# Performance work log

Hardware: AMD Instinct MI355X
Metric: run time of the kernel (lower is better)

## Reference

```python
import jax, jax.numpy as jnp
import numpy as np

B, N, DIM, H, D = 1, 1024, 512, 8, 64
BC, BS, K, W = 16, 16, 8, 256   # compress blk, selection blk, top-k blocks, sliding window
C = N // BC                     # number of compression / selection blocks
SCALE = D ** -0.5
EPS = 1e-6
NEG = -1e30


def rmsnorm(x):
    return x * jax.lax.rsqrt(jnp.mean(x * x, axis=-1, keepdims=True) + EPS)


def rope(x):  # x: [B,H,N,D], GPT-NeoX style half rotation
    half = D // 2
    inv = 1.0 / (10000.0 ** (jnp.arange(half, dtype=jnp.float32) / half))
    ang = jnp.arange(x.shape[2], dtype=jnp.float32)[:, None] * inv
    cos, sin = jnp.cos(ang), jnp.sin(ang)
    x1, x2 = x[..., :half], x[..., half:]
    return jnp.concatenate([x1 * cos - x2 * sin, x2 * cos + x1 * sin], axis=-1).astype(x.dtype)


def setup_inputs():
    key = jax.random.key(0)
    ks = jax.random.split(key, 24)
    w = lambda k, shape, fan: jax.random.normal(k, shape, jnp.float32) * (fan ** -0.5)
    return {
        'x':  jax.random.normal(ks[0], (B, N, DIM), jnp.float32),
        've': jax.random.normal(ks[1], (B, N, DIM), jnp.float32),
        'x0': jax.random.normal(ks[2], (B, N, DIM), jnp.float32),
        'lambdas': jnp.array([1.0, 0.0], jnp.float32),
        'Wq': w(ks[3], (DIM, H * D), DIM),
        'Wk': w(ks[4], (DIM, H * D), DIM),
        'Wv': w(ks[5], (DIM, H * D), DIM),
        'Wo': w(ks[6], (H * D, DIM), H * D),
        'Wg': w(ks[7], (DIM, 3 * H), DIM),
        'k_pos': w(ks[8], (H, BC, D), D),
        'v_pos': w(ks[9], (H, BC, D), D),
        'Wck': w(ks[10], (BC * D, D), BC * D),
        'bck': jnp.zeros((D,), jnp.float32),
        'Wcv': w(ks[11], (BC * D, D), BC * D),
        'bcv': jnp.zeros((D,), jnp.float32),
        'k_mem': w(ks[12], (H, 1, D), D),
        'v_mem': w(ks[13], (H, 1, D), D),
        'W1': w(ks[14], (DIM, 4 * DIM), DIM),
        'W2': w(ks[15], (4 * DIM, DIM), 4 * DIM),
    }


def _nsa_attn(xn, Wq, Wk, Wv, Wo, Wg, k_pos, v_pos, Wck, bck, Wcv, bcv, k_mem, v_mem):
    q = (xn @ Wq).reshape(B, N, H, D).transpose(0, 2, 1, 3)   # [B,H,N,D]
    k = (xn @ Wk).reshape(B, N, H, D).transpose(0, 2, 1, 3)
    v = (xn @ Wv).reshape(B, N, H, D).transpose(0, 2, 1, 3)
    q, k = rope(q), rope(k)
    i_idx = jnp.arange(N)

    # ---- compressed branch: pool kv into blocks via learned linear + intra-block pos emb ----
    kb = k.reshape(B, H, C, BC, D) + k_pos[None, :, None]
    vb = v.reshape(B, H, C, BC, D) + v_pos[None, :, None]
    ck = kb.reshape(B, H, C, BC * D) @ Wck + bck              # [B,H,C,D]
    cv = vb.reshape(B, H, C, BC * D) @ Wcv + bcv
    ckf = jnp.concatenate([jnp.broadcast_to(k_mem[None], (B, H, 1, D)), ck], axis=2)
    cvf = jnp.concatenate([jnp.broadcast_to(v_mem[None], (B, H, 1, D)), cv], axis=2)
    csim = jnp.einsum('bhid,bhjd->bhij', q, ckf) * SCALE      # [B,H,N,C+1]
    past = ((jnp.arange(C) + 1) * BC - 1)[None, :] < i_idx[:, None]   # block fully in the past
    cmask = jnp.concatenate([jnp.ones((N, 1), bool), past], axis=1)   # mem kv always visible
    cattn = jax.nn.softmax(jnp.where(cmask[None, None], csim, NEG), axis=-1)
    c_out = jnp.einsum('bhij,bhjd->bhid', cattn, cvf)

    # ---- fine selection branch: top-K blocks by compressed attention importance ----
    imp = jnp.where(past[None, None], cattn[..., 1:], NEG)    # [B,H,N,C]
    vals, sel = jax.lax.top_k(imp, K)                         # [B,H,N,K]
    valid = vals >= 0.0                                       # drop picks among masked blocks
    kb_f = k.reshape(B, H, C, BS, D)
    vb_f = v.reshape(B, H, C, BS, D)
    k_sel = jnp.take_along_axis(kb_f[:, :, None], sel[..., None, None], axis=3)  # [B,H,N,K,BS,D]
    v_sel = jnp.take_along_axis(vb_f[:, :, None], sel[..., None, None], axis=3)
    own = i_idx // BS                                         # query's own block, causal inside
    k_fine = jnp.concatenate([k_sel, kb_f[:, :, own][:, :, :, None]], axis=3)    # [B,H,N,K+1,BS,D]
    v_fine = jnp.concatenate([v_sel, vb_f[:, :, own][:, :, :, None]], axis=3)
    offs = jnp.arange(BS)
    m_sel = (sel[..., None] * BS + offs <= i_idx[None, None, :, None, None]) & valid[..., None]
    m_own = jnp.broadcast_to((own[:, None] * BS + offs <= i_idx[:, None])[None, None, :, None], (B, H, N, 1, BS))
    m_fine = jnp.concatenate([m_sel, m_own], axis=3)
    fsim = jnp.where(m_fine, jnp.einsum('bhnd,bhnksd->bhnks', q, k_fine) * SCALE, NEG)
    fattn = jax.nn.softmax(fsim.reshape(B, H, N, (K + 1) * BS), axis=-1).reshape(B, H, N, K + 1, BS)
    f_out = jnp.einsum('bhnks,bhnksd->bhnd', fattn, v_fine)

    # ---- sliding window branch ----
    smask = (i_idx[None, :] <= i_idx[:, None]) & (i_idx[:, None] - i_idx[None, :] < W)
    ssim = jnp.where(smask[None, None], jnp.einsum('bhid,bhjd->bhij', q, k) * SCALE, NEG)
    s_out = jnp.einsum('bhij,bhjd->bhid', jax.nn.softmax(ssim, axis=-1), v)

    # ---- per-head sigmoid gates combine the three strategies ----
    gates = jax.nn.sigmoid(xn @ Wg).reshape(B, N, H, 3).transpose(0, 2, 1, 3)  # [B,H,N,3]
    o = gates[..., 0:1] * c_out + gates[..., 1:2] * f_out + gates[..., 2:3] * s_out
    return o.transpose(0, 2, 1, 3).reshape(B, N, H * D) @ Wo


def reference(x, ve, x0, lambdas, Wq, Wk, Wv, Wo, Wg, k_pos, v_pos, Wck, bck, Wcv, bcv, k_mem, v_mem, W1, W2):
    # ve is accepted by NSABlock.forward but never consumed in this block
    x = lambdas[0] * x + lambdas[1] * x0
    x = x + _nsa_attn(rmsnorm(x), Wq, Wk, Wv, Wo, Wg, k_pos, v_pos, Wck, bck, Wcv, bcv, k_mem, v_mem)
    x = x + jnp.square(jax.nn.relu(rmsnorm(x) @ W1)) @ W2
    return x
```

## Files before the change

kernel.cpp:

```cpp
#include <hip/hip_runtime.h>
#include <math.h>

#define NTOK 1024
#define DIMM 512
#define NH 8
#define HD 64
#define BCB 16
#define BSB 16
#define KSEL 8
#define WWIN 256
#define CBLK 64
#define SCALE 0.125f
#define EPSV 1e-6f
#define NEGV -1e30f

typedef short bf16x8 __attribute__((ext_vector_type(8)));
typedef float f32x4 __attribute__((ext_vector_type(4)));

__device__ inline ushort f2b(float f) {
  union { float f; unsigned int u; } c; c.f = f;
  unsigned int u = c.u;
  return (ushort)((u + 0x7FFFu + ((u >> 16) & 1u)) >> 16);
}
__device__ inline float b2f(ushort h) {
  union { unsigned int u; float f; } c; c.u = ((unsigned int)h) << 16;
  return c.f;
}

__device__ inline float wred_max(float v) {
#pragma unroll
  for (int off = 1; off < 64; off <<= 1) v = fmaxf(v, __shfl_xor(v, off));
  return v;
}
__device__ inline float wred_sum(float v) {
#pragma unroll
  for (int off = 1; off < 64; off <<= 1) v += __shfl_xor(v, off);
  return v;
}

struct WtrDesc { const float* src; ushort* dh; ushort* dl; int K; int Nsrc; int Npad; };
struct WtrPack { WtrDesc d[9]; int cum[9]; };

__global__ void __launch_bounds__(256)
k_pre(WtrPack pk, const float* __restrict__ x, const float* __restrict__ x0,
      const float* __restrict__ lam, float* __restrict__ xr,
      ushort* __restrict__ xnh, ushort* __restrict__ xnl) {
  if ((int)blockIdx.x < pk.cum[8]) {
    int gb = blockIdx.x;
    int e = 0;
    while (gb >= pk.cum[e]) e++;
    int start = e ? pk.cum[e - 1] : 0;
    WtrDesc dd = pk.d[e];
    int local = gb - start;
    int XT = dd.Npad >> 5;
    int bx = local % XT, by = local / XT;
    __shared__ float t[32][33];
    int n0 = bx * 32, k0 = by * 32;
    int tx = threadIdx.x & 31, ty = threadIdx.x >> 5;
#pragma unroll
    for (int i = 0; i < 32; i += 8)
      t[ty + i][tx] = (n0 + tx < dd.Nsrc)
          ? dd.src[(size_t)(k0 + ty + i) * dd.Nsrc + n0 + tx] : 0.f;
    __syncthreads();
#pragma unroll
    for (int i = 0; i < 32; i += 8) {
      float vv = t[tx][ty + i];
      ushort h = f2b(vv);
      size_t di = (size_t)(n0 + ty + i) * dd.K + k0 + tx;
      dd.dh[di] = h;
      if (dd.dl) dd.dl[di] = f2b(vv - b2f(h));
    }
  } else {
    int row = blockIdx.x - pk.cum[8], tid = threadIdx.x;
    float l0 = lam[0], l1 = lam[1];
    size_t b = (size_t)row * DIMM;
    float a0 = l0 * x[b + tid]       + l1 * x0[b + tid];
    float a1 = l0 * x[b + tid + 256] + l1 * x0[b + tid + 256];
    xr[b + tid] = a0; xr[b + tid + 256] = a1;
    float ss = a0 * a0 + a1 * a1;
    __shared__ float sm[8];
    for (int o = 32; o > 0; o >>= 1) ss += __shfl_down(ss, o);
    int lane = tid & 63, wid = tid >> 6;
    if (lane == 0) sm[wid] = ss;
    __syncthreads();
    if (tid == 0) {
      float s = sm[0] + sm[1] + sm[2] + sm[3];
      sm[0] = rsqrtf(s / (float)DIMM + EPSV);
    }
    __syncthreads();
    float r = sm[0];
    float v0 = a0 * r, v1 = a1 * r;
    ushort h0 = f2b(v0), h1 = f2b(v1);
    xnh[b + tid] = h0;        xnh[b + tid + 256] = h1;
    xnl[b + tid] = f2b(v0 - b2f(h0));
    xnl[b + tid + 256] = f2b(v1 - b2f(h1));
  }
}

__global__ void __launch_bounds__(256)
k_rms_bf(const float* __restrict__ xr, const float* __restrict__ p0,
         const float* __restrict__ p1, float* __restrict__ outb,
         ushort* __restrict__ y) {
  int row = blockIdx.x, tid = threadIdx.x;
  size_t b = (size_t)row * DIMM;
  float a0 = xr[b + tid]       + p0[b + tid]       + p1[b + tid];
  float a1 = xr[b + tid + 256] + p0[b + tid + 256] + p1[b + tid + 256];
  outb[b + tid] = a0; outb[b + tid + 256] = a1;
  float ss = a0 * a0 + a1 * a1;
  __shared__ float sm[8];
  for (int o = 32; o > 0; o >>= 1) ss += __shfl_down(ss, o);
  int lane = tid & 63, wid = tid >> 6;
  if (lane == 0) sm[wid] = ss;
  __syncthreads();
  if (tid == 0) {
    float s = sm[0] + sm[1] + sm[2] + sm[3];
    sm[0] = rsqrtf(s / (float)DIMM + EPSV);
  }
  __syncthreads();
  float r = sm[0];
  y[b + tid] = f2b(a0 * r); y[b + tid + 256] = f2b(a1 * r);
}

__global__ void __launch_bounds__(256)
k_gemm_w1(const ushort* __restrict__ A, const ushort* __restrict__ BT,
          ushort* __restrict__ Co) {
  const int Kd = 512, Nd = 2048;
  __shared__ ushort As[128 * 40];
  __shared__ ushort Bs[64 * 40];
  int tid = threadIdx.x;
  int lane = tid & 63, w = tid >> 6;
  int rb = blockIdx.y * 128, cb = blockIdx.x * 64;
  int wm = (w >> 1) * 64, wn = (w & 1) * 32;
  int quad = lane >> 4, l15 = lane & 15;
  int srA = tid >> 1, scA = (tid & 1) * 16;
  int srB = tid >> 2, scB = (tid & 3) * 8;

  f32x4 acc[4][2];
#pragma unroll
  for (int i = 0; i < 4; i++)
#pragma unroll
    for (int j = 0; j < 2; j++) acc[i][j] = (f32x4){0.f, 0.f, 0.f, 0.f};

  const ushort* ap = A  + (size_t)(rb + srA) * Kd + scA;
  const ushort* bp = BT + (size_t)(cb + srB) * Kd + scB;
  ushort* aw = &As[srA * 40 + scA];
  ushort* bw = &Bs[srB * 40 + scB];

  int4 pa0 = *(const int4*)ap;
  int4 pa1 = *(const int4*)(ap + 8);
  int4 pb  = *(const int4*)bp;

  for (int k0 = 0; k0 < Kd; k0 += 32) {
    if (k0) __syncthreads();
    *(int4*)aw = pa0; *(int4*)(aw + 8) = pa1;
    *(int4*)bw = pb;
    __syncthreads();
    if (k0 + 32 < Kd) {
      pa0 = *(const int4*)(ap + k0 + 32);
      pa1 = *(const int4*)(ap + k0 + 40);
      pb  = *(const int4*)(bp + k0 + 32);
    }
    bf16x8 af[4], bfr[2];
#pragma unroll
    for (int t = 0; t < 4; t++)
      af[t] = *(const bf16x8*)&As[(wm + t * 16 + l15) * 40 + quad * 8];
#pragma unroll
    for (int t = 0; t < 2; t++)
      bfr[t] = *(const bf16x8*)&Bs[(wn + t * 16 + l15) * 40 + quad * 8];
#pragma unroll
    for (int i = 0; i < 4; i++)
#pragma unroll
      for (int j = 0; j < 2; j++)
        acc[i][j] = __builtin_amdgcn_mfma_f32_16x16x32_bf16(af[i], bfr[j],
                                                            acc[i][j], 0, 0, 0);
  }

#pragma unroll
  for (int i = 0; i < 4; i++) {
#pragma unroll
    for (int j = 0; j < 2; j++) {
      int col = cb + wn + j * 16 + l15;
#pragma unroll
      for (int r = 0; r < 4; r++) {
        int row = rb + wm + i * 16 + quad * 4 + r;
        float t = fmaxf(acc[i][j][r], 0.f);
        Co[(size_t)row * Nd + col] = f2b(t * t);
      }
    }
  }
}

__global__ void __launch_bounds__(256)
k_gemm_w2(const ushort* __restrict__ A, const ushort* __restrict__ BT,
          float* __restrict__ outb) {
  const int Kd = 2048;
  __shared__ ushort As[64 * 40];
  __shared__ ushort Bs[64 * 40];
  int tid = threadIdx.x;
  int lane = tid & 63, w = tid >> 6;
  int rb = blockIdx.y * 64, cb = blockIdx.x * 64;
  int kb = blockIdx.z * 1024;
  int wm = (w >> 1) * 32, wn = (w & 1) * 32;
  int quad = lane >> 4, l15 = lane & 15;
  int srow = tid >> 2, scol = (tid & 3) * 8;

  f32x4 acc[2][2];
#pragma unroll
  for (int i = 0; i < 2; i++)
#pragma unroll
    for (int j = 0; j < 2; j++) acc[i][j] = (f32x4){0.f, 0.f, 0.f, 0.f};

  const ushort* ap = A  + (size_t)(rb + srow) * Kd + kb + scol;
  const ushort* bp = BT + (size_t)(cb + srow) * Kd + kb + scol;
  ushort* aw = &As[srow * 40 + scol];
  ushort* bw = &Bs[srow * 40 + scol];

  int4 pa = *(const int4*)ap;
  int4 pb = *(const int4*)bp;

  for (int k0 = 0; k0 < 1024; k0 += 32) {
    if (k0) __syncthreads();
    *(int4*)aw = pa;
    *(int4*)bw = pb;
    __syncthreads();
    if (k0 + 32 < 1024) {
      pa = *(const int4*)(ap + k0 + 32);
      pb = *(const int4*)(bp + k0 + 32);
    }
    bf16x8 af[2], bfr[2];
#pragma unroll
    for (int t = 0; t < 2; t++) {
      af[t]  = *(const bf16x8*)&As[(wm + t * 16 + l15) * 40 + quad * 8];
      bfr[t] = *(const bf16x8*)&Bs[(wn + t * 16 + l15) * 40 + quad * 8];
    }
#pragma unroll
    for (int i = 0; i < 2; i++)
#pragma unroll
      for (int j = 0; j < 2; j++)
        acc[i][j] = __builtin_amdgcn_mfma_f32_16x16x32_bf16(af[i], bfr[j],
                                                            acc[i][j], 0, 0, 0);
  }

#pragma unroll
  for (int i = 0; i < 2; i++) {
#pragma unroll
    for (int j = 0; j < 2; j++) {
      int col = cb + wn + j * 16 + l15;
#pragma unroll
      for (int r = 0; r < 4; r++) {
        int row = rb + wm + i * 16 + quad * 4 + r;
        atomicAdd(&outb[(size_t)row * 512 + col], acc[i][j][r]);
      }
    }
  }
}

__global__ void __launch_bounds__(256)
k_gemm_wo(const float* __restrict__ cg, const float* __restrict__ fg,
          const float* __restrict__ sg, const float* __restrict__ gates,
          const ushort* __restrict__ BT, float* __restrict__ P0,
          float* __restrict__ P1) {
  __shared__ ushort As[64 * 40];
  __shared__ ushort Bs[64 * 40];
  int tid = threadIdx.x;
  int lane = tid & 63, wave = tid >> 6;
  int rb = blockIdx.y * 64, cb = blockIdx.x * 64;
  int kb = blockIdx.z * 256;
  int wm = (wave >> 1) * 32, wn = (wave & 1) * 32;
  int q = lane >> 4, l15 = lane & 15;
  int srow = tid >> 2, scol = (tid & 3) * 8;

  f32x4 acc[2][2];
#pragma unroll
  for (int i = 0; i < 2; i++)
#pragma unroll
    for (int j = 0; j < 2; j++) acc[i][j] = (f32x4){0.f, 0.f, 0.f, 0.f};

  int row = rb + srow;
  const ushort* bp = BT + (size_t)(cb + srow) * 512 + kb + scol;
  ushort* aw = &As[srow * 40 + scol];
  ushort* bw = &Bs[srow * 40 + scol];

  for (int k0 = 0; k0 < 256; k0 += 32) {
    int colb = kb + k0 + scol;
    int hh = colb >> 6;
    const float* gp = gates + (size_t)row * 24 + hh * 3;
    float g0 = gp[0], g1 = gp[1], g2 = gp[2];
    size_t off = (size_t)row * 512 + colb;
    float4 c0 = *(const float4*)(cg + off), c1 = *(const float4*)(cg + off + 4);
    float4 f0 = *(const float4*)(fg + off), f1 = *(const float4*)(fg + off + 4);
    float4 s0 = *(const float4*)(sg + off), s1 = *(const float4*)(sg + off + 4);
    float va[8] = {g0 * c0.x + g1 * f0.x + g2 * s0.x,
                   g0 * c0.y + g1 * f0.y + g2 * s0.y,
                   g0 * c0.z + g1 * f0.z + g2 * s0.z,
                   g0 * c0.w + g1 * f0.w + g2 * s0.w,
                   g0 * c1.x + g1 * f1.x + g2 * s1.x,
                   g0 * c1.y + g1 * f1.y + g2 * s1.y,
                   g0 * c1.z + g1 * f1.z + g2 * s1.z,
                   g0 * c1.w + g1 * f1.w + g2 * s1.w};
    ushort h[8];
#pragma unroll
    for (int e = 0; e < 8; e++) h[e] = f2b(va[e]);
    *(int4*)aw = *(int4*)h;
    *(int4*)bw = *(const int4*)(bp + k0);
    __syncthreads();
    bf16x8 af[2], bfr[2];
#pragma unroll
    for (int t = 0; t < 2; t++) {
      af[t]  = *(const bf16x8*)&As[(wm + t * 16 + l15) * 40 + q * 8];
      bfr[t] = *(const bf16x8*)&Bs[(wn + t * 16 + l15) * 40 + q * 8];
    }
#pragma unroll
    for (int i = 0; i < 2; i++)
#pragma unroll
      for (int j = 0; j < 2; j++)
        acc[i][j] = __builtin_amdgcn_mfma_f32_16x16x32_bf16(af[i], bfr[j],
                                                            acc[i][j], 0, 0, 0);
    __syncthreads();
  }

  float* pbuf = blockIdx.z ? P1 : P0;
#pragma unroll
  for (int i = 0; i < 2; i++) {
#pragma unroll
    for (int j = 0; j < 2; j++) {
      int col = cb + wn + j * 16 + l15;
#pragma unroll
      for (int r = 0; r < 4; r++) {
        int rr = rb + wm + i * 16 + q * 4 + r;
        pbuf[(size_t)rr * 512 + col] = acc[i][j][r];
      }
    }
  }
}

__global__ void __launch_bounds__(256)
k_gemm_qkv(const ushort* __restrict__ Ah, const ushort* __restrict__ Al,
           const ushort* __restrict__ BTh, const ushort* __restrict__ BTl,
           float* __restrict__ Co, float* __restrict__ vhm,
           float* __restrict__ gates, int Kd) {
  __shared__ ushort Ash[64 * 40];
  __shared__ ushort Asl[64 * 40];
  __shared__ ushort Bsh[64 * 40];
  __shared__ ushort Bsl[64 * 40];
  int tid = threadIdx.x;
  int lane = tid & 63, wave = tid >> 6;
  int rb = blockIdx.y * 64, cb = blockIdx.x * 64;
  const bool prec = (cb < 1024);
  int wm = (wave >> 1) * 32, wn = (wave & 1) * 32;
  int q = lane >> 4, l15 = lane & 15;
  int srow = tid >> 2, scol = (tid & 3) * 8;

  f32x4 acc[2][2];
#pragma unroll
  for (int i = 0; i < 2; i++)
#pragma unroll
    for (int j = 0; j < 2; j++) acc[i][j] = (f32x4){0.f, 0.f, 0.f, 0.f};

  const ushort* aph = Ah  + (size_t)(rb + srow) * Kd + scol;
  const ushort* apl = Al  + (size_t)(rb + srow) * Kd + scol;
  const ushort* bph = BTh + (size_t)(cb + srow) * Kd + scol;
  const ushort* bpl = BTl + (size_t)(cb + srow) * Kd + scol;
  ushort* awh = &Ash[srow * 40 + scol];
  ushort* awl = &Asl[srow * 40 + scol];
  ushort* bwh = &Bsh[srow * 40 + scol];
  ushort* bwl = &Bsl[srow * 40 + scol];

  for (int k0 = 0; k0 < Kd; k0 += 32) {
    *(int4*)awh = *(const int4*)(aph + k0);
    *(int4*)bwh = *(const int4*)(bph + k0);
    if (prec) {
      *(int4*)awl = *(const int4*)(apl + k0);
      *(int4*)bwl = *(const int4*)(bpl + k0);
    }
    __syncthreads();
    bf16x8 afh[2], afl[2], bfh[2], bfl[2];
#pragma unroll
    for (int t = 0; t < 2; t++) {
      int ar = (wm + t * 16 + l15) * 40 + q * 8;
      int br = (wn + t * 16 + l15) * 40 + q * 8;
      afh[t] = *(const bf16x8*)&Ash[ar];
      bfh[t] = *(const bf16x8*)&Bsh[br];
      if (prec) {
        afl[t] = *(const bf16x8*)&Asl[ar];
        bfl[t] = *(const bf16x8*)&Bsl[br];
      }
    }
#pragma unroll
    for (int i = 0; i < 2; i++)
#pragma unroll
      for (int j = 0; j < 2; j++) {
        acc[i][j] = __builtin_amdgcn_mfma_f32_16x16x32_bf16(afh[i], bfh[j],
                                                            acc[i][j], 0, 0, 0);
        if (prec) {
          acc[i][j] = __builtin_amdgcn_mfma_f32_16x16x32_bf16(afh[i], bfl[j],
                                                              acc[i][j], 0, 0, 0);
          acc[i][j] = __builtin_amdgcn_mfma_f32_16x16x32_bf16(afl[i], bfh[j],
                                                              acc[i][j], 0, 0, 0);
        }
      }
    __syncthreads();
  }

  const size_t NW = (size_t)NTOK * DIMM;
#pragma unroll
  for (int i = 0; i < 2; i++) {
#pragma unroll
    for (int j = 0; j < 2; j++) {
      int col = cb + wn + j * 16 + l15;
#pragma unroll
      for (int r = 0; r < 4; r++) {
        int row = rb + wm + i * 16 + q * 4 + r;
        float vv = acc[i][j][r];
        if (cb >= 1536) {
          int c24 = col - 1536;
          if (c24 < 24)
            gates[(size_t)row * 24 + c24] = 1.f / (1.f + expf(-vv));
        } else if (col >= 1024) {
          int c = col - 1024;
          vhm[(size_t)(c >> 6) * 65536 + (size_t)row * 64 + (c & 63)] = vv;
        } else {
          Co[(size_t)(col >> 9) * NW + (size_t)row * 512 + (col & 511)] = vv;
        }
      }
    }
  }
}

__global__ void __launch_bounds__(256)
k_rope(float* __restrict__ q, const float* __restrict__ k,
       float* __restrict__ khm, ushort* __restrict__ khm_bf,
       const float* __restrict__ vhm, ushort* __restrict__ vhm_bf) {
  int idx = blockIdx.x * 256 + threadIdx.x;
  int seg = idx >> 18;
  if (seg >= 2) {
    int ci = idx - 524288;
    if (ci < 131072) {
      float4 t = *(const float4*)(vhm + (size_t)ci * 4);
      ushort4 u = {f2b(t.x), f2b(t.y), f2b(t.z), f2b(t.w)};
      *(ushort4*)(vhm_bf + (size_t)ci * 4) = u;
    }
    return;
  }
  int r = idx & 262143;
  int j = r & 31;
  int h = (r >> 5) & 7;
  int n = r >> 8;
  float inv = powf(10000.f, -(float)j / 32.f);
  float ang = (float)n * inv;
  float sn, cs;
  sincosf(ang, &sn, &cs);
  size_t base = (size_t)n * DIMM + h * HD + j;
  if (seg == 0) {
    float x1 = q[base], x2 = q[base + 32];
    q[base] = x1 * cs - x2 * sn;
    q[base + 32] = x2 * cs + x1 * sn;
  } else {
    float x1 = k[base], x2 = k[base + 32];
    float o1 = x1 * cs - x2 * sn;
    float o2 = x2 * cs + x1 * sn;
    size_t ob = (size_t)h * 65536 + (size_t)n * 64 + j;
    khm[ob] = o1;
    khm[ob + 32] = o2;
    khm_bf[ob] = f2b(o1);
    khm_bf[ob + 32] = f2b(o2);
  }
}

__global__ void __launch_bounds__(256)
k_mid(const float* __restrict__ khm, const float* __restrict__ vhm,
      const float* __restrict__ k_pos, const float* __restrict__ v_pos,
      const ushort* __restrict__ WckTh, const ushort* __restrict__ WckTl,
      const ushort* __restrict__ WcvTh, const ushort* __restrict__ WcvTl,
      const float* __restrict__ bck, const float* __restrict__ bcv,
      float* __restrict__ ckb, float* __restrict__ cvb,
      const float* __restrict__ qg, const ushort* __restrict__ khm_bf,
      const ushort* __restrict__ vhm_bf, float* __restrict__ sout) {
  __shared__ union {
    struct { ushort Ash[32 * 72]; ushort Asl[32 * 72];
             ushort Bsh[64 * 72]; ushort Bsl[64 * 72]; } c;
    struct { ushort Kt[64 * 72]; ushort VT[64 * 72];
             ushort Qs[64 * 72]; ushort Ps[4][16 * 72]; } s;
  } U;
  int tid = threadIdx.x, lane = tid & 63, w = tid >> 6;
  int quad = lane >> 4, l15 = lane & 15;

  if (blockIdx.x < 32) {
    int h = blockIdx.x & 7, kv = (blockIdx.x >> 3) & 1, mh = blockIdx.x >> 4;
    const float* src = kv ? vhm : khm;
    const float* pos = kv ? v_pos : k_pos;
    const ushort* WTh = kv ? WcvTh : WckTh;
    const ushort* WTl = kv ? WcvTl : WckTl;
    const float* bias = kv ? bcv : bck;
    float* outp = kv ? cvb : ckb;

    ushort* Ash = U.c.Ash; ushort* Asl = U.c.Asl;
    ushort* Bsh = U.c.Bsh; ushort* Bsl = U.c.Bsl;
    int wmi = w >> 1, wnj = w & 1;
    int arow = tid >> 3, ae0 = (tid & 7) * 8;
    int brow = tid >> 2, be0 = (tid & 3) * 16;

    f32x4 acc[2];
#pragma unroll
    for (int j = 0; j < 2; j++) acc[j] = (f32x4){0.f, 0.f, 0.f, 0.f};

    for (int t = 0; t < 16; t++) {
      const float* ar = src + (size_t)h * 65536 +
                        (size_t)((mh * 32 + arow) * 16 + t) * 64 + ae0;
      const float* pr = pos + (size_t)(h * 16 + t) * HD + ae0;
      ushort hh[8], hl[8];
#pragma unroll
      for (int u = 0; u < 2; u++) {
        float4 av = *(const float4*)(ar + u * 4);
        float4 pv = *(const float4*)(pr + u * 4);
        float vals[4] = {av.x + pv.x, av.y + pv.y, av.z + pv.z, av.w + pv.w};
#pragma unroll
        for (int e = 0; e < 4; e++) {
          ushort hb = f2b(vals[e]);
          hh[u * 4 + e] = hb;
          hl[u * 4 + e] = f2b(vals[e] - b2f(hb));
        }
      }
      *(int4*)&Ash[arow * 72 + ae0] = *(int4*)hh;
      *(int4*)&Asl[arow * 72 + ae0] = *(int4*)hl;
      const ushort* bh = WTh + (size_t)brow * 1024 + t * 64 + be0;
      const ushort* bl = WTl + (size_t)brow * 1024 + t * 64 + be0;
      *(int4*)&Bsh[brow * 72 + be0]     = *(const int4*)bh;
      *(int4*)&Bsh[brow * 72 + be0 + 8] = *(const int4*)(bh + 8);
      *(int4*)&Bsl[brow * 72 + be0]     = *(const int4*)bl;
      *(int4*)&Bsl[brow * 72 + be0 + 8] = *(const int4*)(bl + 8);
      __syncthreads();
#pragma unroll
      for (int sub = 0; sub < 2; sub++) {
        int ar2 = (wmi * 16 + l15) * 72 + sub * 32 + quad * 8;
        bf16x8 afh = *(const bf16x8*)&Ash[ar2];
        bf16x8 afl = *(const bf16x8*)&Asl[ar2];
#pragma unroll
        for (int j = 0; j < 2; j++) {
          int br2 = (wnj * 32 + j * 16 + l15) * 72 + sub * 32 + quad * 8;
          bf16x8 bfh = *(const bf16x8*)&Bsh[br2];
          bf16x8 bfl = *(const bf16x8*)&Bsl[br2];
          acc[j] = __builtin_amdgcn_mfma_f32_16x16x32_bf16(afh, bfh, acc[j], 0, 0, 0);
          acc[j] = __builtin_amdgcn_mfma_f32_16x16x32_bf16(afh, bfl, acc[j], 0, 0, 0);
          acc[j] = __builtin_amdgcn_mfma_f32_16x16x32_bf16(afl, bfh, acc[j], 0, 0, 0);
        }
      }
      __syncthreads();
    }

#pragma unroll
    for (int j = 0; j < 2; j++) {
      int d = wnj * 32 + j * 16 + l15;
      float bv = bias[d];
#pragma unroll
      for (int r = 0; r < 4; r++) {
        int c = mh * 32 + wmi * 16 + quad * 4 + r;
        outp[((size_t)h * 64 + c) * 64 + d] = acc[j][r] + bv;
      }
    }
  } else {
    int sidx = blockIdx.x - 32;
    int h = sidx >> 4, i0 = (sidx & 15) * 64;
    ushort* Kt = U.s.Kt; ushort* VT = U.s.VT; ushort* Qs = U.s.Qs;

#pragma unroll
    for (int it = 0; it < 2; it++) {
      int f = it * 256 + tid;
      int r = f >> 3, d0 = (f & 7) * 8;
      const float* qp = qg + (size_t)(i0 + r) * DIMM + h * HD + d0;
      float4 t0 = *(const float4*)qp;
      float4 t1 = *(const float4*)(qp + 4);
      ushort u[8] = {f2b(t0.x), f2b(t0.y), f2b(t0.z), f2b(t0.w),
                     f2b(t1.x), f2b(t1.y), f2b(t1.z), f2b(t1.w)};
      *(int4*)&Qs[r * 72 + d0] = *(int4*)u;
    }

    int lo = i0 - (WWIN - 1); if (lo < 0) lo = 0;
    int jb_lo = lo >> 6, jb_hi = (i0 + 63) >> 6;

    float mrow[4], lrow[4];
    f32x4 Of[4];
#pragma unroll
    for (int r = 0; r < 4; r++) { mrow[r] = NEGV; lrow[r] = 0.f; }
#pragma unroll
    for (int d = 0; d < 4; d++) Of[d] = (f32x4){0.f, 0.f, 0.f, 0.f};

    for (int jb = jb_lo; jb <= jb_hi; jb++) {
      __syncthreads();
#pragma unroll
      for (int it = 0; it < 2; it++) {
        int f = it * 256 + tid;
        int r = f >> 3, c8 = (f & 7) * 8;
        const ushort* kp = khm_bf + (size_t)h * 65536 + (size_t)(jb * 64 + r) * 64 + c8;
        *(int4*)&Kt[r * 72 + c8] = *(const int4*)kp;
        const ushort* vp = vhm_bf + (size_t)h * 65536 + (size_t)(jb * 64 + r) * 64 + c8;
        ushort vv[8];
        *(int4*)vv = *(const int4*)vp;
#pragma unroll
        for (int e = 0; e < 8; e++) VT[(c8 + e) * 72 + r] = vv[e];
      }
      __syncthreads();

      bf16x8 qa[2];
#pragma unroll
      for (int c = 0; c < 2; c++)
        qa[c] = *(const bf16x8*)&Qs[(w * 16 + l15) * 72 + c * 32 + quad * 8];

      f32x4 sc[4];
#pragma unroll
      for (int ks = 0; ks < 4; ks++) {
        f32x4 a = (f32x4){0.f, 0.f, 0.f, 0.f};
#pragma unroll
        for (int c = 0; c < 2; c++) {
          bf16x8 kb = *(const bf16x8*)&Kt[(ks * 16 + l15) * 72 + c * 32 + quad * 8];
          a = __builtin_amdgcn_mfma_f32_16x16x32_bf16(qa[c], kb, a, 0, 0, 0);
        }
        sc[ks] = a;
      }

      float pm[4][4], rmax[4];
#pragma unroll
      for (int r = 0; r < 4; r++) rmax[r] = NEGV;
#pragma unroll
      for (int ks = 0; ks < 4; ks++) {
        int gj = jb * 64 + ks * 16 + l15;
#pragma unroll
        for (int r = 0; r < 4; r++) {
          int qi = i0 + w * 16 + quad * 4 + r;
          bool vis = (gj <= qi) && (qi - gj < WWIN);
          float s = vis ? sc[ks][r] * SCALE : NEGV;
          pm[ks][r] = s;
          rmax[r] = fmaxf(rmax[r], s);
        }
      }
#pragma unroll
      for (int off = 1; off < 16; off <<= 1)
#pragma unroll
        for (int r = 0; r < 4; r++)
          rmax[r] = fmaxf(rmax[r], __shfl_xor(rmax[r], off));

      float alpha[4], rsum[4];
#pragma unroll
      for (int r = 0; r < 4; r++) {
        float newm = fmaxf(mrow[r], rmax[r]);
        alpha[r] = expf(mrow[r] - newm);
        mrow[r] = newm;
        rsum[r] = 0.f;
      }
#pragma unroll
      for (int ks = 0; ks < 4; ks++)
#pragma unroll
        for (int r = 0; r < 4; r++) {
          float p = expf(pm[ks][r] - mrow[r]);
          pm[ks][r] = p;
          rsum[r] += p;
        }
#pragma unroll
      for (int off = 1; off < 16; off <<= 1)
#pragma unroll
        for (int r = 0; r < 4; r++)
          rsum[r] += __shfl_xor(rsum[r], off);
#pragma unroll
      for (int r = 0; r < 4; r++)
        lrow[r] = lrow[r] * alpha[r] + rsum[r];

#pragma unroll
      for (int ks = 0; ks < 4; ks++)
#pragma unroll
        for (int r = 0; r < 4; r++)
          U.s.Ps[w][(quad * 4 + r) * 72 + ks * 16 + l15] = f2b(pm[ks][r]);
#pragma unroll
      for (int d = 0; d < 4; d++)
#pragma unroll
        for (int r = 0; r < 4; r++)
          Of[d][r] *= alpha[r];

#pragma unroll
      for (int c = 0; c < 2; c++) {
        bf16x8 pa = *(const bf16x8*)&U.s.Ps[w][l15 * 72 + c * 32 + quad * 8];
#pragma unroll
        for (int d = 0; d < 4; d++) {
          bf16x8 vb = *(const bf16x8*)&VT[(d * 16 + l15) * 72 + c * 32 + quad * 8];
          Of[d] = __builtin_amdgcn_mfma_f32_16x16x32_bf16(pa, vb, Of[d], 0, 0, 0);
        }
      }
    }

#pragma unroll
    for (int d = 0; d < 4; d++)
#pragma unroll
      for (int r = 0; r < 4; r++) {
        int qi = i0 + w * 16 + quad * 4 + r;
        sout[(size_t)qi * DIMM + h * HD + d * 16 + l15] = Of[d][r] / lrow[r];
      }
  }
}

__global__ void __launch_bounds__(256)
k_cmp(const float* __restrict__ qg, const float* __restrict__ ckb,
      const float* __restrict__ cvb, const float* __restrict__ k_mem,
      const float* __restrict__ v_mem, float* __restrict__ cout,
      int* __restrict__ sel) {
  int h = blockIdx.y, i0 = blockIdx.x * 16;
  int tid = threadIdx.x, lane = tid & 63, w = tid >> 6;
  __shared__ float ckt[64][65];
  __shared__ float cvs[64][65];
  __shared__ float qs[16][64];
  __shared__ float kms[64], vms[64];
  __shared__ float sp[4][64];

#pragma unroll
  for (int r = 0; r < 4; r++) {
    int f = r * 256 + tid;
    int c = f >> 4, d0 = (f & 15) * 4;
    float4 t = *(const float4*)(ckb + ((size_t)h * 64 + c) * 64 + d0);
    ckt[d0][c] = t.x; ckt[d0 + 1][c] = t.y; ckt[d0 + 2][c] = t.z; ckt[d0 + 3][c] = t.w;
    float4 u = *(const float4*)(cvb + ((size_t)h * 64 + c) * 64 + d0);
    cvs[c][d0] = u.x; cvs[c][d0 + 1] = u.y; cvs[c][d0 + 2] = u.z; cvs[c][d0 + 3] = u.w;
  }
  {
    int r = tid >> 4, d0 = (tid & 15) * 4;
    float4 t = *(const float4*)(qg + (size_t)(i0 + r) * DIMM + h * HD + d0);
    qs[r][d0] = t.x; qs[r][d0 + 1] = t.y; qs[r][d0 + 2] = t.z; qs[r][d0 + 3] = t.w;
  }
  if (tid < 64) kms[tid] = k_mem[h * HD + tid];
  else if (tid < 128) vms[tid - 64] = v_mem[h * HD + tid - 64];
  __syncthreads();

  for (int s = 0; s < 4; s++) {
    int ql = w * 4 + s, qi = i0 + ql;
    float dot = 0.f, dm = 0.f;
#pragma unroll 8
    for (int e = 0; e < 64; e++) {
      float qe = qs[ql][e];
      dot = fmaf(qe, ckt[e][lane], dot);
      dm  = fmaf(qe, kms[e], dm);
    }
    bool vis = (lane * BCB + BCB - 1) < qi;
    float sj = vis ? dot * SCALE : NEGV;
    float smem = dm * SCALE;
    float m = wred_max(fmaxf(sj, smem));
    float p = expf(sj - m);
    float pmem = expf(smem - m);
    float l = wred_sum(p) + pmem;
    float inv = 1.f / l;

    float impv = vis ? p : NEGV;
#pragma unroll
    for (int kk = 0; kk < KSEL; kk++) {
      float bv = impv; int bi = lane;
#pragma unroll
      for (int off = 32; off > 0; off >>= 1) {
        float ov = __shfl_xor(bv, off);
        int   oi = __shfl_xor(bi, off);
        if (ov > bv || (ov == bv && oi < bi)) { bv = ov; bi = oi; }
      }
      if (lane == 0) sel[((size_t)h * NTOK + qi) * KSEL + kk] = (bv >= 0.f) ? bi : -1;
      if (lane == bi) impv = NEGV;
    }

    sp[w][lane] = p;
    float od = pmem * vms[lane];
#pragma unroll 8
    for (int j = 0; j < 64; j++) od = fmaf(sp[w][j], cvs[j][lane], od);
    cout[(size_t)qi * DIMM + h * HD + lane] = od * inv;
  }
}

__global__ void __launch_bounds__(256)
k_fine(const float* __restrict__ qg, const ushort* __restrict__ khm_bf,
       const ushort* __restrict__ vhm_bf, const int* __restrict__ sel,
       float* __restrict__ fout) {
  int i = blockIdx.x, h = blockIdx.y;
  int tid = threadIdx.x, lane = tid & 63, w = tid >> 6;
  __shared__ float qsh[64];
  __shared__ ushort vsb[144 * 64];
  __shared__ float sp[144];
  __shared__ int selS[8];
  __shared__ float mred[4], sredS[4];
  __shared__ float pacc[4][64];

  int own = i >> 4;
  if (tid < 64) qsh[tid] = qg[(size_t)i * DIMM + h * HD + tid];
  if (tid >= 64 && tid < 72)
    selS[tid - 64] = sel[((size_t)h * NTOK + i) * KSEL + tid - 64];
  __syncthreads();

  const ushort* kbase = khm_bf + (size_t)h * 65536;
  const ushort* vbase = vhm_bf + (size_t)h * 65536;

#pragma unroll
  for (int it = 0; it < 5; it++) {
    int idx = it * 256 + tid;
    if (idx < 1152) {
      int row = idx >> 3, c8 = (idx & 7) * 8;
      int kk = row >> 4;
      int bidx = (kk < KSEL) ? selS[kk] : own;
      if (bidx < 0) bidx = 0;
      *(int4*)&vsb[row * 64 + c8] =
          *(const int4*)(vbase + (size_t)(bidx * BSB + (row & 15)) * 64 + c8);
    }
  }

  float s_loc = NEGV;
  bool active = (tid < 144);
  if (active) {
    int kk = tid >> 4;
    int bidx; bool vis;
    if (kk < KSEL) {
      bidx = selS[kk];
      vis = (bidx >= 0);
      if (!vis) bidx = 0;
    } else {
      bidx = own;
      vis = (tid - 128) <= (i & 15);
    }
    const ushort* kr = kbase + (size_t)(bidx * BSB + (tid & 15)) * 64;
    float dot = 0.f;
#pragma unroll
    for (int e8 = 0; e8 < 8; e8++) {
      ushort kv[8];
      *(int4*)kv = *(const int4*)(kr + e8 * 8);
#pragma unroll
      for (int e = 0; e < 8; e++)
        dot = fmaf(qsh[e8 * 8 + e], b2f(kv[e]), dot);
    }
    s_loc = vis ? dot * SCALE : NEGV;
  }
  float mw = wred_max(s_loc);
  if (lane == 0) mred[w] = mw;
  __syncthreads();
  float m = fmaxf(fmaxf(mred[0], mred[1]), fmaxf(mred[2], mred[3]));
  float p = active ? expf(s_loc - m) : 0.f;
  float sw = wred_sum(p);
  if (lane == 0) sredS[w] = sw;
  if (active) sp[tid] = p;
  __syncthreads();
  float l = sredS[0] + sredS[1] + sredS[2] + sredS[3];

  float acc = 0.f;
  int j0 = w * 36;
#pragma unroll 6
  for (int jj = 0; jj < 36; jj++) {
    int j = j0 + jj;
    acc = fmaf(sp[j], b2f(vsb[j * 64 + lane]), acc);
  }
  pacc[w][lane] = acc;
  __syncthreads();
  if (w == 0)
    fout[(size_t)i * DIMM + h * HD + lane] =
        (pacc[0][lane] + pacc[1][lane] + pacc[2][lane] + pacc[3][lane]) / l;
}

extern "C" void kernel_launch(void* const* d_in, const int* in_sizes, int n_in,
                              void* d_out, int out_size, void* d_ws, size_t ws_size,
                              hipStream_t stream) {
  const float* x     = (const float*)d_in[0];
  const float* ve    = (const float*)d_in[1]; (void)ve;
  const float* x0    = (const float*)d_in[2];
  const float* lam   = (const float*)d_in[3];
  const float* Wq    = (const float*)d_in[4];
  const float* Wk    = (const float*)d_in[5];
  const float* Wv    = (const float*)d_in[6];
  const float* Wo    = (const float*)d_in[7];
  const float* Wg    = (const float*)d_in[8];
  const float* k_pos = (const float*)d_in[9];
  const float* v_pos = (const float*)d_in[10];
  const float* Wck   = (const float*)d_in[11];
  const float* bck   = (const float*)d_in[12];
  const float* Wcv   = (const float*)d_in[13];
  const float* bcv   = (const float*)d_in[14];
  const float* k_mem = (const float*)d_in[15];
  const float* v_mem = (const float*)d_in[16];
  const float* W1    = (const float*)d_in[17];
  const float* W2    = (const float*)d_in[18];
  float* out = (float*)d_out;
  float* ws  = (float*)d_ws;

  const size_t NW = (size_t)NTOK * DIMM;
  float* xr    = ws;
  float* xn    = ws + 1 * NW;
  float* q     = ws + 2 * NW;
  float* k     = ws + 3 * NW;
  float* vhm   = ws + 4 * NW;
  float* coutb = ws + 5 * NW;
  float* foutb = ws + 6 * NW;
  float* soutb = ws + 7 * NW;
  float* khm   = ws + 8 * NW;
  float* gates = ws + 9 * NW;
  float* ckb   = gates + 32768;
  float* cvb   = ckb + 32768;
  int*   selb  = (int*)(cvb + 32768);
  ushort* qkvTh = (ushort*)(cvb + 32768 + 65536);
  ushort* qkvTl = qkvTh + 1600 * 512;
  ushort* WoT   = qkvTl + 1600 * 512;
  ushort* W1T   = WoT   + 512 * 512;
  ushort* W2T   = W1T   + 2048 * 512;
  ushort* WckTh = W2T   + 512 * 2048;
  ushort* WckTl = WckTh + 64 * 1024;
  ushort* WcvTh = WckTl + 64 * 1024;
  ushort* WcvTl = WcvTh + 64 * 1024;
  float* p0w = k;
  float* p1w = q;
  ushort* ybf = (ushort*)soutb;
  ushort* h1b = (ushort*)q;
  ushort* xnh = (ushort*)xn;
  ushort* xnl = xnh + NW;
  ushort* khm_bf = (ushort*)xn;
  ushort* vhm_bf = khm_bf + 524288;

  WtrPack pk;
  pk.d[0] = {Wq, qkvTh,              qkvTl,              512, 512,  512};
  pk.d[1] = {Wk, qkvTh + 512 * 512,  qkvTl + 512 * 512,  512, 512,  512};
  pk.d[2] = {Wv, qkvTh + 1024 * 512, qkvTl + 1024 * 512, 512, 512,  512};
  pk.d[3] = {Wo, WoT, nullptr,  512, 512,  512};
  pk.d[4] = {W1, W1T, nullptr,  512, 2048, 2048};
  pk.d[5] = {W2, W2T, nullptr, 2048, 512,  512};
  pk.d[6] = {Wck, WckTh, WckTl, 1024, 64, 64};
  pk.d[7] = {Wcv, WcvTh, WcvTl, 1024, 64, 64};
  pk.d[8] = {Wg, qkvTh + 1536 * 512, qkvTl + 1536 * 512, 512, 24, 64};
  int cum = 0;
  for (int e = 0; e < 9; e++) {
    cum += (pk.d[e].Npad / 32) * (pk.d[e].K / 32);
    pk.cum[e] = cum;
  }

  k_pre<<<cum + NTOK, 256, 0, stream>>>(pk, x, x0, lam, xr, xnh, xnl);

  k_gemm_qkv<<<dim3(25, NTOK / 64), 256, 0, stream>>>(
      xnh, xnl, qkvTh, qkvTl, q, vhm, gates, 512);
  k_rope<<<2560, 256, 0, stream>>>(q, k, khm, khm_bf, vhm, vhm_bf);

  k_mid<<<160, 256, 0, stream>>>(khm, vhm, k_pos, v_pos,
                                 WckTh, WckTl, WcvTh, WcvTl,
                                 bck, bcv, ckb, cvb,
                                 q, khm_bf, vhm_bf, soutb);

  k_cmp<<<dim3(NTOK / 16, NH), 256, 0, stream>>>(q, ckb, cvb, k_mem, v_mem,
                                                 coutb, selb);
  k_fine<<<dim3(NTOK, NH), 256, 0, stream>>>(q, khm_bf, vhm_bf, selb, foutb);

  k_gemm_wo<<<dim3(512 / 64, NTOK / 64, 2), 256, 0, stream>>>(
      coutb, foutb, soutb, gates, WoT, p0w, p1w);
  k_rms_bf<<<NTOK, 256, 0, stream>>>(xr, p0w, p1w, out, ybf);

  k_gemm_w1<<<dim3(2048 / 64, NTOK / 128), 256, 0, stream>>>(ybf, W1T, h1b);
  k_gemm_w2<<<dim3(512 / 64, NTOK / 64, 2), 256, 0, stream>>>(h1b, W2T, out);
}
```

Before: 246.2 us.

## Fuse RoPE and bf16 split into QKV GEMM epilogue, precompute pos-emb projection

Removes the separate k_rope kernel. RoPE is now applied in the QKV GEMM epilogue through a shared-memory staging tile and precomputed cos/sin tables, and K/V are written directly as hi/lo bf16 pairs in head-major layout. The compression branch's positional-embedding contribution (pos @ W + bias) is computed once in k_pre and added as a per-head bias, so k_mid loads bf16 hi/lo directly instead of converting fp32 each tile. This cuts one launch and the fp32 intermediate traffic, at the cost of a heavier GEMM epilogue with an extra barrier and a serial 256-iteration dot loop in a few k_pre blocks.

Measured after the change: 250.8 us. About the same (+1.9%).

```diff
diff --git a/kernel.cpp b/kernel.cpp
--- a/kernel.cpp
+++ b/kernel.cpp
@@ -44,9 +44,18 @@
 __global__ void __launch_bounds__(256)
 k_pre(WtrPack pk, const float* __restrict__ x, const float* __restrict__ x0,
       const float* __restrict__ lam, float* __restrict__ xr,
-      ushort* __restrict__ xnh, ushort* __restrict__ xnl) {
-  if ((int)blockIdx.x < pk.cum[8]) {
-    int gb = blockIdx.x;
+      ushort* __restrict__ xnh, ushort* __restrict__ xnl,
+      float* __restrict__ ctab, float* __restrict__ stab,
+      const float* __restrict__ k_pos, const float* __restrict__ v_pos,
+      const float* __restrict__ Wck, const float* __restrict__ Wcv,
+      const float* __restrict__ bck, const float* __restrict__ bcv,
+      float* __restrict__ pwk, float* __restrict__ pwv) {
+  __shared__ float t[32][33];
+  __shared__ float sm[8];
+  __shared__ float red[4][64];
+  int bid = blockIdx.x, tid = threadIdx.x;
+  if (bid < pk.cum[8]) {
+    int gb = bid;
     int e = 0;
     while (gb >= pk.cum[e]) e++;
     int start = e ? pk.cum[e - 1] : 0;
@@ -54,9 +63,8 @@
     int local = gb - start;
     int XT = dd.Npad >> 5;
     int bx = local % XT, by = local / XT;
-    __shared__ float t[32][33];
     int n0 = bx * 32, k0 = by * 32;
-    int tx = threadIdx.x & 31, ty = threadIdx.x >> 5;
+    int tx = tid & 31, ty = tid >> 5;
 #pragma unroll
     for (int i = 0; i < 32; i += 8)
       t[ty + i][tx] = (n0 + tx < dd.Nsrc)
@@ -70,15 +78,14 @@
       dd.dh[di] = h;
       if (dd.dl) dd.dl[di] = f2b(vv - b2f(h));
     }
-  } else {
-    int row = blockIdx.x - pk.cum[8], tid = threadIdx.x;
+  } else if (bid < pk.cum[8] + NTOK) {
+    int row = bid - pk.cum[8];
     float l0 = lam[0], l1 = lam[1];
     size_t b = (size_t)row * DIMM;
     float a0 = l0 * x[b + tid]       + l1 * x0[b + tid];
     float a1 = l0 * x[b + tid + 256] + l1 * x0[b + tid + 256];
     xr[b + tid] = a0; xr[b + tid + 256] = a1;
     float ss = a0 * a0 + a1 * a1;
-    __shared__ float sm[8];
     for (int o = 32; o > 0; o >>= 1) ss += __shfl_down(ss, o);
     int lane = tid & 63, wid = tid >> 6;
     if (lane == 0) sm[wid] = ss;
@@ -94,6 +101,30 @@
     xnh[b + tid] = h0;        xnh[b + tid + 256] = h1;
     xnl[b + tid] = f2b(v0 - b2f(h0));
     xnl[b + tid + 256] = f2b(v1 - b2f(h1));
+  } else if (bid < pk.cum[8] + NTOK + 128) {
+    int g = (bid - pk.cum[8] - NTOK) * 256 + tid;
+    int n = g >> 5, d = g & 31;
+    float inv = powf(10000.f, -(float)d / 32.f);
+    float sn, cs;
+    sincosf((float)n * inv, &sn, &cs);
+    ctab[g] = cs; stab[g] = sn;
+  } else {
+    int idx2 = bid - pk.cum[8] - NTOK - 128;
+    int h = idx2 & 7, kv = idx2 >> 3;
+    const float* pos = kv ? v_pos : k_pos;
+    const float* W = kv ? Wcv : Wck;
+    const float* bias = kv ? bcv : bck;
+    float* pw = kv ? pwv : pwk;
+    int d = tid & 63, part = tid >> 6;
+    float s = 0.f;
+    for (int i = 0; i < 256; i++) {
+      int kk = part * 256 + i;
+      s += pos[h * 1024 + kk] * W[(size_t)kk * 64 + d];
+    }
+    red[part][d] = s;
+    __syncthreads();
+    if (part == 0)
+      pw[h * 64 + d] = red[0][d] + red[1][d] + red[2][d] + red[3][d] + bias[d];
   }
 }
 
@@ -337,12 +368,16 @@
 __global__ void __launch_bounds__(256)
 k_gemm_qkv(const ushort* __restrict__ Ah, const ushort* __restrict__ Al,
            const ushort* __restrict__ BTh, const ushort* __restrict__ BTl,
-           float* __restrict__ Co, float* __restrict__ vhm,
-           float* __restrict__ gates, int Kd) {
-  __shared__ ushort Ash[64 * 40];
-  __shared__ ushort Asl[64 * 40];
-  __shared__ ushort Bsh[64 * 40];
-  __shared__ ushort Bsl[64 * 40];
+           float* __restrict__ qout, ushort* __restrict__ khm_h,
+           ushort* __restrict__ khm_l, ushort* __restrict__ vhm_h,
+           ushort* __restrict__ vhm_l, float* __restrict__ gates,
+           const float* __restrict__ ctab, const float* __restrict__ stab,
+           int Kd) {
+  __shared__ ushort SM[4 * 64 * 40];
+  ushort* Ash = SM;
+  ushort* Asl = SM + 2560;
+  ushort* Bsh = SM + 5120;
+  ushort* Bsl = SM + 7680;
   int tid = threadIdx.x;
   int lane = tid & 63, wave = tid >> 6;
   int rb = blockIdx.y * 64, cb = blockIdx.x * 64;
@@ -402,25 +437,59 @@
     __syncthreads();
   }
 
-  const size_t NW = (size_t)NTOK * DIMM;
-#pragma unroll
-  for (int i = 0; i < 2; i++) {
-#pragma unroll
-    for (int j = 0; j < 2; j++) {
-      int col = cb + wn + j * 16 + l15;
-#pragma unroll
-      for (int r = 0; r < 4; r++) {
-        int row = rb + wm + i * 16 + q * 4 + r;
-        float vv = acc[i][j][r];
-        if (cb >= 1536) {
-          int c24 = col - 1536;
-          if (c24 < 24)
-            gates[(size_t)row * 24 + c24] = 1.f / (1.f + expf(-vv));
-        } else if (col >= 1024) {
-          int c = col - 1024;
-          vhm[(size_t)(c >> 6) * 65536 + (size_t)row * 64 + (c & 63)] = vv;
-        } else {
-          Co[(size_t)(col >> 9) * NW + (size_t)row * 512 + (col & 511)] = vv;
+  if (cb < 1024) {
+    float* st = (float*)SM;
+#pragma unroll
+    for (int i = 0; i < 2; i++)
+#pragma unroll
+      for (int j = 0; j < 2; j++)
+#pragma unroll
+        for (int r = 0; r < 4; r++)
+          st[(wm + i * 16 + q * 4 + r) * 66 + wn + j * 16 + l15] = acc[i][j][r];
+    __syncthreads();
+    int h = (cb & 511) >> 6;
+#pragma unroll
+    for (int e = 0; e < 8; e++) {
+      int p = e * 256 + tid;
+      int rw = p >> 5, d = p & 31;
+      int n = rb + rw;
+      float x1 = st[rw * 66 + d], x2 = st[rw * 66 + d + 32];
+      float cs = ctab[n * 32 + d], sn = stab[n * 32 + d];
+      float o1 = x1 * cs - x2 * sn;
+      float o2 = x2 * cs + x1 * sn;
+      if (cb < 512) {
+        qout[(size_t)n * 512 + h * 64 + d]      = o1;
+        qout[(size_t)n * 512 + h * 64 + d + 32] = o2;
+      } else {
+        size_t ob = (size_t)h * 65536 + (size_t)n * 64 + d;
+        ushort b1 = f2b(o1), b2v = f2b(o2);
+        khm_h[ob]      = b1;
+        khm_h[ob + 32] = b2v;
+        khm_l[ob]      = f2b(o1 - b2f(b1));
+        khm_l[ob + 32] = f2b(o2 - b2f(b2v));
+      }
+    }
+  } else {
+#pragma unroll
+    for (int i = 0; i < 2; i++) {
+#pragma unroll
+      for (int j = 0; j < 2; j++) {
+        int col = cb + wn + j * 16 + l15;
+#pragma unroll
+        for (int r = 0; r < 4; r++) {
+          int row = rb + wm + i * 16 + q * 4 + r;
+          float vv = acc[i][j][r];
+          if (cb >= 1536) {
+            int c24 = col - 1536;
+            if (c24 < 24)
+              gates[(size_t)row * 24 + c24] = 1.f / (1.f + expf(-vv));
+          } else {
+            int c = col - 1024;
+            size_t ob = (size_t)(c >> 6) * 65536 + (size_t)row * 64 + (c & 63);
+            ushort hb = f2b(vv);
+            vhm_h[ob] = hb;
+            vhm_l[ob] = f2b(vv - b2f(hb));
+          }
         }
       }
     }
@@ -428,54 +497,13 @@
 }
 
 __global__ void __launch_bounds__(256)
-k_rope(float* __restrict__ q, const float* __restrict__ k,
-       float* __restrict__ khm, ushort* __restrict__ khm_bf,
-       const float* __restrict__ vhm, ushort* __restrict__ vhm_bf) {
-  int idx = blockIdx.x * 256 + threadIdx.x;
-  int seg = idx >> 18;
-  if (seg >= 2) {
-    int ci = idx - 524288;
-    if (ci < 131072) {
-      float4 t = *(const float4*)(vhm + (size_t)ci * 4);
-      ushort4 u = {f2b(t.x), f2b(t.y), f2b(t.z), f2b(t.w)};
-      *(ushort4*)(vhm_bf + (size_t)ci * 4) = u;
-    }
-    return;
-  }
-  int r = idx & 262143;
-  int j = r & 31;
-  int h = (r >> 5) & 7;
-  int n = r >> 8;
-  float inv = powf(10000.f, -(float)j / 32.f);
-  float ang = (float)n * inv;
-  float sn, cs;
-  sincosf(ang, &sn, &cs);
-  size_t base = (size_t)n * DIMM + h * HD + j;
-  if (seg == 0) {
-    float x1 = q[base], x2 = q[base + 32];
-    q[base] = x1 * cs - x2 * sn;
-    q[base + 32] = x2 * cs + x1 * sn;
-  } else {
-    float x1 = k[base], x2 = k[base + 32];
-    float o1 = x1 * cs - x2 * sn;
-    float o2 = x2 * cs + x1 * sn;
-    size_t ob = (size_t)h * 65536 + (size_t)n * 64 + j;
-    khm[ob] = o1;
-    khm[ob + 32] = o2;
-    khm_bf[ob] = f2b(o1);
-    khm_bf[ob + 32] = f2b(o2);
-  }
-}
-
-__global__ void __launch_bounds__(256)
-k_mid(const float* __restrict__ khm, const float* __restrict__ vhm,
-      const float* __restrict__ k_pos, const float* __restrict__ v_pos,
+k_mid(const ushort* __restrict__ khm_h, const ushort* __restrict__ khm_l,
+      const ushort* __restrict__ vhm_h, const ushort* __restrict__ vhm_l,
       const ushort* __restrict__ WckTh, const ushort* __restrict__ WckTl,
       const ushort* __restrict__ WcvTh, const ushort* __restrict__ WcvTl,
-      const float* __restrict__ bck, const float* __restrict__ bcv,
+      const float* __restrict__ pwk, const float* __restrict__ pwv,
       float* __restrict__ ckb, float* __restrict__ cvb,
-      const float* __restrict__ qg, const ushort* __restrict__ khm_bf,
-      const ushort* __restrict__ vhm_bf, float* __restrict__ sout) {
+      const float* __restrict__ qg, float* __restrict__ sout) {
   __shared__ union {
     struct { ushort Ash[32 * 72]; ushort Asl[32 * 72];
              ushort Bsh[64 * 72]; ushort Bsl[64 * 72]; } c;
@@ -487,11 +515,11 @@
 
   if (blockIdx.x < 32) {
     int h = blockIdx.x & 7, kv = (blockIdx.x >> 3) & 1, mh = blockIdx.x >> 4;
-    const float* src = kv ? vhm : khm;
-    const float* pos = kv ? v_pos : k_pos;
+    const ushort* sH = kv ? vhm_h : khm_h;
+    const ushort* sL = kv ? vhm_l : khm_l;
     const ushort* WTh = kv ? WcvTh : WckTh;
     const ushort* WTl = kv ? WcvTl : WckTl;
-    const float* bias = kv ? bcv : bck;
+    const float* pw = (kv ? pwv : pwk) + h * 64;
     float* outp = kv ? cvb : ckb;
 
     ushort* Ash = U.c.Ash; ushort* Asl = U.c.Asl;
@@ -499,36 +527,21 @@
     int wmi = w >> 1, wnj = w & 1;
     int arow = tid >> 3, ae0 = (tid & 7) * 8;
     int brow = tid >> 2, be0 = (tid & 3) * 16;
+    size_t abase = (size_t)h * 65536 + (size_t)(mh * 32 + arow) * 1024 + ae0;
+    size_t bbase = (size_t)brow * 1024 + be0;
 
     f32x4 acc[2];
 #pragma unroll
     for (int j = 0; j < 2; j++) acc[j] = (f32x4){0.f, 0.f, 0.f, 0.f};
 
     for (int t = 0; t < 16; t++) {
-      const float* ar = src + (size_t)h * 65536 +
-                        (size_t)((mh * 32 + arow) * 16 + t) * 64 + ae0;
-      const float* pr = pos + (size_t)(h * 16 + t) * HD + ae0;
-      ushort hh[8], hl[8];
-#pragma unroll
-      for (int u = 0; u < 2; u++) {
-        float4 av = *(const float4*)(ar + u * 4);
-        float4 pv = *(const float4*)(pr + u * 4);
-        float vals[4] = {av.x + pv.x, av.y + pv.y, av.z + pv.z, av.w + pv.w};
-#pragma unroll
-        for (int e = 0; e < 4; e++) {
-          ushort hb = f2b(vals[e]);
-          hh[u * 4 + e] = hb;
-          hl[u * 4 + e] = f2b(vals[e] - b2f(hb));
-        }
-      }
-      *(int4*)&Ash[arow * 72 + ae0] = *(int4*)hh;
-      *(int4*)&Asl[arow * 72 + ae0] = *(int4*)hl;
-      const ushort* bh = WTh + (size_t)brow * 1024 + t * 64 + be0;
-      const ushort* bl = WTl + (size_t)brow * 1024 + t * 64 + be0;
-      *(int4*)&Bsh[brow * 72 + be0]     = *(const int4*)bh;
-      *(int4*)&Bsh[brow * 72 + be0 + 8] = *(const int4*)(bh + 8);
-      *(int4*)&Bsl[brow * 72 + be0]     = *(const int4*)bl;
-      *(int4*)&Bsl[brow * 72 + be0 + 8] = *(const int4*)(bl + 8);
+      int kb = t * 64;
+      *(int4*)&Ash[arow * 72 + ae0] = *(const int4*)(sH + abase + kb);
+      *(int4*)&Asl[arow * 72 + ae0] = *(const int4*)(sL + abase + kb);
+      *(int4*)&Bsh[brow * 72 + be0]     = *(const int4*)(WTh + bbase + kb);
+      *(int4*)&Bsh[brow * 72 + be0 + 8] = *(const int4*)(WTh + bbase + kb + 8);
+      *(int4*)&Bsl[brow * 72 + be0]     = *(const int4*)(WTl + bbase + kb);
+      *(int4*)&Bsl[brow * 72 + be0 + 8] = *(const int4*)(WTl + bbase + kb + 8);
       __syncthreads();
 #pragma unroll
       for (int sub = 0; sub < 2; sub++) {
@@ -551,7 +564,7 @@
 #pragma unroll
     for (int j = 0; j < 2; j++) {
       int d = wnj * 32 + j * 16 + l15;
-      float bv = bias[d];
+      float bv = pw[d];
 #pragma unroll
       for (int r = 0; r < 4; r++) {
         int c = mh * 32 + wmi * 16 + quad * 4 + r;
@@ -591,9 +604,9 @@
       for (int it = 0; it < 2; it++) {
         int f = it * 256 + tid;
         int r = f >> 3, c8 = (f & 7) * 8;
-        const ushort* kp = khm_bf + (size_t)h * 65536 + (size_t)(jb * 64 + r) * 64 + c8;
+        const ushort* kp = khm_h + (size_t)h * 65536 + (size_t)(jb * 64 + r) * 64 + c8;
         *(int4*)&Kt[r * 72 + c8] = *(const int4*)kp;
-        const ushort* vp = vhm_bf + (size_t)h * 65536 + (size_t)(jb * 64 + r) * 64 + c8;
+        const ushort* vp = vhm_h + (size_t)h * 65536 + (size_t)(jb * 64 + r) * 64 + c8;
         ushort vv[8];
         *(int4*)vv = *(const int4*)vp;
 #pragma unroll
@@ -881,12 +894,11 @@
   float* xr    = ws;
   float* xn    = ws + 1 * NW;
   float* q     = ws + 2 * NW;
-  float* k     = ws + 3 * NW;
-  float* vhm   = ws + 4 * NW;
+  float* kslot = ws + 3 * NW;
+  float* vslot = ws + 4 * NW;
   float* coutb = ws + 5 * NW;
   float* foutb = ws + 6 * NW;
   float* soutb = ws + 7 * NW;
-  float* khm   = ws + 8 * NW;
   float* gates = ws + 9 * NW;
   float* ckb   = gates + 32768;
   float* cvb   = ckb + 32768;
@@ -900,14 +912,21 @@
   ushort* WckTl = WckTh + 64 * 1024;
   ushort* WcvTh = WckTl + 64 * 1024;
   ushort* WcvTl = WcvTh + 64 * 1024;
-  float* p0w = k;
+  float* ctab   = (float*)(WcvTl + 64 * 1024);
+  float* stab   = ctab + 32768;
+  float* pwk    = stab + 32768;
+  float* pwv    = pwk + 512;
+
+  ushort* xnh = (ushort*)xn;
+  ushort* xnl = xnh + NW;
+  ushort* khm_h = (ushort*)kslot;
+  ushort* khm_l = khm_h + 524288;
+  ushort* vhm_h = (ushort*)vslot;
+  ushort* vhm_l = vhm_h + 524288;
+  float* p0w = kslot;
   float* p1w = q;
   ushort* ybf = (ushort*)soutb;
   ushort* h1b = (ushort*)q;
-  ushort* xnh = (ushort*)xn;
-  ushort* xnl = xnh + NW;
-  ushort* khm_bf = (ushort*)xn;
-  ushort* vhm_bf = khm_bf + 524288;
 
   WtrPack pk;
   pk.d[0] = {Wq, qkvTh,              qkvTl,              512, 512,  512};
@@ -925,20 +944,21 @@
     pk.cum[e] = cum;
   }
 
-  k_pre<<<cum + NTOK, 256, 0, stream>>>(pk, x, x0, lam, xr, xnh, xnl);
+  k_pre<<<cum + NTOK + 128 + 16, 256, 0, stream>>>(
+      pk, x, x0, lam, xr, xnh, xnl, ctab, stab,
+      k_pos, v_pos, Wck, Wcv, bck, bcv, pwk, pwv);
 
   k_gemm_qkv<<<dim3(25, NTOK / 64), 256, 0, stream>>>(
-      xnh, xnl, qkvTh, qkvTl, q, vhm, gates, 512);
-  k_rope<<<2560, 256, 0, stream>>>(q, k, khm, khm_bf, vhm, vhm_bf);
-
-  k_mid<<<160, 256, 0, stream>>>(khm, vhm, k_pos, v_pos,
+      xnh, xnl, qkvTh, qkvTl, q, khm_h, khm_l, vhm_h, vhm_l, gates,
+      ctab, stab, 512);
+
+  k_mid<<<160, 256, 0, stream>>>(khm_h, khm_l, vhm_h, vhm_l,
                                  WckTh, WckTl, WcvTh, WcvTl,
-                                 bck, bcv, ckb, cvb,
-                                 q, khm_bf, vhm_bf, soutb);
+                                 pwk, pwv, ckb, cvb, q, soutb);
 
   k_cmp<<<dim3(NTOK / 16, NH), 256, 0, stream>>>(q, ckb, cvb, k_mem, v_mem,
                                                  coutb, selb);
-  k_fine<<<dim3(NTOK, NH), 256, 0, stream>>>(q, khm_bf, vhm_bf, selb, foutb);
+  k_fine<<<dim3(NTOK, NH), 256, 0, stream>>>(q, khm_h, vhm_h, selb, foutb);
 
   k_gemm_wo<<<dim3(512 / 64, NTOK / 64, 2), 256, 0, stream>>>(
       coutb, foutb, soutb, gates, WoT, p0w, p1w);
```
